# Performance work log

Hardware: AMD Instinct MI355X
Metric: run time of the kernel (lower is better)

Reference implementation:

```python
import jax, jax.numpy as jnp
import numpy as np
import math

C = 256
N_HEAD = 8
GROUPS = 16
EPS = 1e-5


def group_norm(x, w, b):
    # x: [B, C, H, W]; biased variance over (group_channels, H, W), like torch GroupNorm
    B, Cc, H, W = x.shape
    xg = x.reshape(B, GROUPS, Cc // GROUPS, H, W)
    mean = xg.mean(axis=(2, 3, 4), keepdims=True)
    var = ((xg - mean) ** 2).mean(axis=(2, 3, 4), keepdims=True)
    xn = ((xg - mean) * jax.lax.rsqrt(var + EPS)).reshape(B, Cc, H, W)
    return xn * w[None, :, None, None] + b[None, :, None, None]


def setup_inputs() -> dict:
    key = jax.random.key(0)
    k0, k1, k2, k3, k4, k5 = jax.random.split(key, 6)
    B, H, W = 4, 48, 48
    input_feat = jax.random.normal(k0, (B, C, H, W), dtype=jnp.float32)
    gn_weight = jnp.ones((C,), dtype=jnp.float32) + 0.02 * jax.random.normal(k1, (C,), dtype=jnp.float32)
    gn_bias = 0.02 * jax.random.normal(k2, (C,), dtype=jnp.float32)
    w_qkv = jax.random.normal(k3, (3 * C, C), dtype=jnp.float32) / math.sqrt(C)  # Conv2d 1x1, no bias
    w_out = jax.random.normal(k4, (C, C), dtype=jnp.float32) / math.sqrt(C)      # Conv2d 1x1
    b_out = 0.02 * jax.random.normal(k5, (C,), dtype=jnp.float32)
    return {"input_feat": input_feat, "gn_weight": gn_weight, "gn_bias": gn_bias,
            "w_qkv": w_qkv, "w_out": w_out, "b_out": b_out}


def reference(input_feat, gn_weight, gn_bias, w_qkv, w_out, b_out):
    # H=W=48 <= max_attn_size=48 -> full attention branch
    B, Cc, H, W = input_feat.shape
    n, d = N_HEAD, Cc // N_HEAD
    S = H * W
    normed = group_norm(input_feat, gn_weight, gn_bias)
    # 1x1 conv QKV: [B, 3C, H, W]
    qkv = jnp.einsum('oc,bchw->bohw', w_qkv, normed)
    # view(B, n, 3*d, H, W).chunk(3, dim=2) == reshape to (B, n, 3, d, S)
    qkv = qkv.reshape(B, n, 3, d, S)
    q, k, v = qkv[:, :, 0], qkv[:, :, 1], qkv[:, :, 2]  # each [B, n, d, S]
    # NOTE: original divides by sqrt(channel), not sqrt(head_dim)
    scale = 1.0 / math.sqrt(Cc)
    scores = jnp.einsum('bnds,bndt->bnst', q, k) * scale  # [B, n, S, S]
    attn = jax.nn.softmax(scores, axis=-1)
    o = jnp.einsum('bnst,bndt->bnds', attn, v)  # [B, n, d, S]
    o = o.reshape(B, Cc, H, W)
    out = jnp.einsum('oc,bchw->bohw', w_out, o) + b_out[None, :, None, None]
    return out + input_feat
```

## Files before the change

kernel.cpp:

```cpp
#include <hip/hip_runtime.h>
#include <hip/hip_bf16.h>
#include <stdint.h>

#define S    2304
#define CHN  256
#define BATCH 4
#define NKEYS 1152
#define QS   0.09016844005556021f

typedef __attribute__((ext_vector_type(8))) short bf16x8;
typedef __attribute__((ext_vector_type(4))) short bf16x4;
typedef __attribute__((ext_vector_type(4))) float f32x4;
typedef __attribute__((ext_vector_type(4))) uint32_t u32x4;
typedef __attribute__((ext_vector_type(4))) unsigned short u16x4;
typedef unsigned short u16;

#define AS1 __attribute__((address_space(1)))
#define AS3 __attribute__((address_space(3)))
#define GLDS(gptr, lptr) __builtin_amdgcn_global_load_lds((const AS1 void*)(gptr), (AS3 void*)(lptr), 16, 0, 0)

__device__ __forceinline__ u16 f2bf(float f) {
  union { float f; uint32_t u; } v; v.f = f;
  uint32_t u = v.u;
  u += 0x7fffu + ((u >> 16) & 1u);
  return (u16)(u >> 16);
}
__device__ __forceinline__ float bf2f(u16 h) {
  union { uint32_t u; float f; } v; v.u = ((uint32_t)h) << 16;
  return v.f;
}
__device__ __forceinline__ uint32_t pk_bf16(float a, float b) {
  union { __hip_bfloat162 h; uint32_t u; } cv;
  cv.h = __float22bfloat162_rn(make_float2(a, b));
  return cv.u;
}

__global__ void k_gnstats(const float* __restrict__ x,
                          const float* __restrict__ wq, const float* __restrict__ wo,
                          u16* __restrict__ wq_bf, u16* __restrict__ wo_bf,
                          float* __restrict__ sraw) {
  int blk = blockIdx.x;
  int bg = blk >> 2, part = blk & 3;
  const float4* p = (const float4*)(x + (size_t)bg * 36864) + part * 2304;
  float s = 0.f, ss = 0.f;
  for (int i = threadIdx.x; i < 2304; i += 256) {
    float4 v = p[i];
    s  += v.x + v.y + v.z + v.w;
    ss += v.x * v.x + v.y * v.y + v.z * v.z + v.w * v.w;
  }
  int lane = threadIdx.x & 63, wv = threadIdx.x >> 6;
  for (int m = 1; m < 64; m <<= 1) { s += __shfl_xor(s, m, 64); ss += __shfl_xor(ss, m, 64); }
  __shared__ float rs[4], rss[4];
  if (lane == 0) { rs[wv] = s; rss[wv] = ss; }
  __syncthreads();
  if (threadIdx.x == 0) {
    sraw[blk * 2]     = rs[0] + rs[1] + rs[2] + rs[3];
    sraw[blk * 2 + 1] = rss[0] + rss[1] + rss[2] + rss[3];
  }
  int gid = blk * 256 + threadIdx.x;
  #pragma unroll
  for (int it = 0; it < 3; ++it) {
    int i = gid + it * 65536;
    wq_bf[i] = f2bf(wq[i]);
  }
  wo_bf[gid] = f2bf(wo[gid]);
}

__global__ void k_gnnorm(const float* __restrict__ x, const float* __restrict__ w,
                         const float* __restrict__ bias, const float* __restrict__ sraw,
                         u16* __restrict__ nt) {
  int bid = blockIdx.x;
  int b = bid / 144, r = bid % 144;
  int sblk = r >> 2, cq = r & 3;
  int t = threadIdx.x;
  int ni = t & 63, cgrp = t >> 6;
  int s = sblk * 64 + ni;
  int cbase = cq * 64 + cgrp * 16;
  int bgi = b * 16 + (cbase >> 4);
  float sx  = sraw[bgi * 8]     + sraw[bgi * 8 + 2] + sraw[bgi * 8 + 4] + sraw[bgi * 8 + 6];
  float ssx = sraw[bgi * 8 + 1] + sraw[bgi * 8 + 3] + sraw[bgi * 8 + 5] + sraw[bgi * 8 + 7];
  float mean = sx * (1.f / 36864.f);
  float var  = ssx * (1.f / 36864.f) - mean * mean;
  float rstd = rsqrtf(var + 1e-5f);
  bf16x8 v0, v1;
  #pragma unroll
  for (int e = 0; e < 16; ++e) {
    int c = cbase + e;
    float val = x[(size_t)(b * 256 + c) * S + s];
    float xn = (val - mean) * rstd * w[c] + bias[c];
    if (e < 8) v0[e] = (short)f2bf(xn); else v1[e - 8] = (short)f2bf(xn);
  }
  u16* dst = nt + (size_t)(b * S + s) * 256 + cbase;
  *(bf16x8*)dst = v0;
  *(bf16x8*)(dst + 8) = v1;
}

__global__ __launch_bounds__(256) void k_qkv(const u16* __restrict__ A,
                                             const u16* __restrict__ Bm,
                                             u16* __restrict__ qkt,
                                             u16* __restrict__ vt) {
  __shared__ __align__(16) u16 As[2][64 * 32];
  __shared__ __align__(16) u16 Bs[2][128 * 32];
  int tid = threadIdx.x, lane = tid & 63, w = tid >> 6;
  int wr = w >> 1, wc = w & 1;
  int cb = lane & 15, q4 = lane >> 4;
  int m0 = blockIdx.y * 64, n0 = blockIdx.x * 128;

  const u16* gA0 = A  + (size_t)(m0 + (tid >> 2)) * 256 + (tid & 3) * 8;
  const u16* gB0 = Bm + (size_t)(n0 + (tid >> 2)) * 256 + (tid & 3) * 8;
  const u16* gB1 = gB0 + 64 * 256;
  char* lA = (char*)&As[0][0] + (w << 10);
  char* lB = (char*)&Bs[0][0] + (w << 10);

  #define STAGE_Q(buf, k0) do {                      \
    GLDS(gA0 + (k0), lA + (buf) * 4096);             \
    GLDS(gB0 + (k0), lB + (buf) * 8192);             \
    GLDS(gB1 + (k0), lB + (buf) * 8192 + 4096);      \
  } while (0)

  f32x4 zero4 = {0.f, 0.f, 0.f, 0.f};
  f32x4 acc[2][4];
  for (int i = 0; i < 2; ++i) for (int j = 0; j < 4; ++j) acc[i][j] = zero4;

  STAGE_Q(0, 0);
  __syncthreads();
  for (int ks = 0; ks < 8; ++ks) {
    int cur = ks & 1;
    if (ks < 7) STAGE_Q(cur ^ 1, (ks + 1) * 32);
    const u16* as = &As[cur][0];
    const u16* bs = &Bs[cur][0];
    bf16x8 af[2], bfr[4];
    for (int i = 0; i < 2; ++i)
      af[i]  = *(const bf16x8*)&as[(wr * 32 + i * 16 + cb) * 32 + 8 * q4];
    for (int j = 0; j < 4; ++j)
      bfr[j] = *(const bf16x8*)&bs[(wc * 64 + j * 16 + cb) * 32 + 8 * q4];
    for (int i = 0; i < 2; ++i)
      for (int j = 0; j < 4; ++j)
        acc[i][j] = __builtin_amdgcn_mfma_f32_16x16x32_bf16(af[i], bfr[j], acc[i][j], 0, 0, 0);
    __syncthreads();
  }

  for (int i = 0; i < 2; ++i)
    for (int j = 0; j < 4; ++j) {
      int ob = m0 + wr * 32 + i * 16 + q4 * 4;
      int n  = n0 + wc * 64 + j * 16 + cb;
      int h = ob / 96, oq = ob % 96;
      if (oq < 64) {
        float sc = (oq < 32) ? QS : 1.f;
        u16x4 pk;
        for (int r = 0; r < 4; ++r) pk[r] = f2bf(acc[i][j][r] * sc);
        *(u16x4*)&qkt[(size_t)n * 512 + h * 64 + oq] = pk;
      } else {
        int nk = n & 31;
        int np = (n & ~31) | ((((nk >> 2) & 3) << 3) + ((nk >> 4) << 2) + (nk & 3));
        for (int r = 0; r < 4; ++r)
          vt[(size_t)(h * 32 + oq - 64 + r) * 9216 + np] = f2bf(acc[i][j][r]);
      }
    }
  #undef STAGE_Q
}

__global__ __launch_bounds__(256, 4) void k_attn(const u16* __restrict__ qkt,
                                                 const u16* __restrict__ vt,
                                                 u16* __restrict__ ot) {
  __shared__ __align__(16) u16 Ks[2][2][2048];
  __shared__ __align__(16) u16 Vd[2][2][2048];

  int tid = threadIdx.x, lane = tid & 63, w = tid >> 6;
  int cb = lane & 15, g4 = lane >> 4;
  int qw = w & 1, half = w >> 1;
  int hw = blockIdx.x;
  int orig = (hw & 7) * 144 + (hw >> 3);
  int bh = orig / 36, qtile = orig % 36;
  int b = bh >> 3, h = bh & 7;
  int q0 = qtile * 64 + qw * 32;

  const u16* kbase = qkt + (size_t)(b * S) * 512 + h * 64 + 32 + (size_t)half * NKEYS * 512;
  const u16* vbase = vt + (size_t)(h * 32) * 9216 + (size_t)b * S + half * NKEYS;

  bf16x8 qf[2];
  #pragma unroll
  for (int qi = 0; qi < 2; ++qi)
    qf[qi] = *(const bf16x8*)&qkt[(size_t)(b * S + q0 + 16 * qi + cb) * 512 + h * 64 + 8 * g4];
  bf16x8 vones;
  #pragma unroll
  for (int e = 0; e < 8; ++e) vones[e] = (short)0x3F80;

  f32x4 zero4 = {0.f, 0.f, 0.f, 0.f};
  f32x4 acc_o[2][2];
  acc_o[0][0] = zero4; acc_o[0][1] = zero4; acc_o[1][0] = zero4; acc_o[1][1] = zero4;
  f32x4 lacc4[2]; lacc4[0] = zero4; lacc4[1] = zero4;

  int xk = (cb ^ (cb >> 2)) & 3;

  const u16* p_k = &Ks[half][0][cb * 32 + ((g4 ^ xk) * 8)];
  const u16* p_v[2];
  #pragma unroll
  for (int kk = 0; kk < 2; ++kk)
    p_v[kk] = &Vd[half][0][cb * 64 + (((4 * kk + g4) ^ (cb & 7)) << 3)];

  int ww = w & 1;
  int c1 = ww * 64 + lane, c2 = c1 + 128;
  int kr1 = c1 >> 2, kc1 = (c1 & 3) ^ ((kr1 ^ (kr1 >> 2)) & 3);
  int kr2 = c2 >> 2, kc2 = (c2 & 3) ^ ((kr2 ^ (kr2 >> 2)) & 3);
  int vr1 = c1 >> 3, vc1 = (c1 & 7) ^ (vr1 & 7);
  int vr2 = c2 >> 3, vc2 = (c2 & 7) ^ (vr2 & 7);
  const u16* gK1 = kbase + (size_t)kr1 * 512 + kc1 * 8;
  const u16* gK2 = kbase + (size_t)kr2 * 512 + kc2 * 8;
  const u16* gV1 = vbase + (size_t)vr1 * 9216 + vc1 * 8;
  const u16* gV2 = vbase + (size_t)vr2 * 9216 + vc2 * 8;
  char* ldsK = (char*)&Ks[half][0][0] + (ww << 10);
  char* ldsV = (char*)&Vd[half][0][0] + (ww << 10);

  #define STAGE_A(buf) do {                          \
    GLDS(gK1, ldsK + (buf) * 4096);                  \
    GLDS(gK2, ldsK + (buf) * 4096 + 2048);           \
    GLDS(gV1, ldsV + (buf) * 4096);                  \
    GLDS(gV2, ldsV + (buf) * 4096 + 2048);           \
    gK1 += 64 * 512; gK2 += 64 * 512;                \
    gV1 += 64; gV2 += 64;                            \
  } while (0)

  #define TILE(buf, pf) do {                                                   \
    if (pf) STAGE_A(buf ^ 1);                                                  \
    bf16x8 kf[4];                                                              \
    _Pragma("unroll")                                                          \
    for (int k4 = 0; k4 < 4; ++k4)                                             \
      kf[k4] = *(const bf16x8*)(p_k + (buf) * 2048 + k4 * 512);                \
    bf16x8 vb[2][2];                          \
    _Pragma("unroll")                                                          \
    for (int jd = 0; jd < 2; ++jd)                                             \
      _Pragma("unroll")                                                        \
      for (int kk = 0; kk < 2; ++kk)                                           \
        vb[jd][kk] = *(const bf16x8*)(p_v[kk] + (buf) * 2048 + jd * 1024);     \
    _Pragma("unroll")                                                          \
    for (int qi = 0; qi < 2; ++qi) {                                           \
      f32x4 pacc[4];                                                           \
      __builtin_amdgcn_s_setprio(1);                                           \
      _Pragma("unroll")                                                        \
      for (int k4 = 0; k4 < 4; ++k4)                                           \
        pacc[k4] = __builtin_amdgcn_mfma_f32_16x16x32_bf16(kf[k4], qf[qi], zero4, 0, 0, 0); \
      __builtin_amdgcn_s_setprio(0);                                           \
      uint32_t W01[4], W23[4];                                                 \
      _Pragma("unroll")                                                        \
      for (int k4 = 0; k4 < 4; ++k4) {                                         \
        f32x4 p = pacc[k4];                                                    \
        float e0 = __builtin_amdgcn_exp2f(p[0]);                               \
        float e1 = __builtin_amdgcn_exp2f(p[1]);                               \
        float e2 = __builtin_amdgcn_exp2f(p[2]);                               \
        float e3 = __builtin_amdgcn_exp2f(p[3]);                               \
        W01[k4] = pk_bf16(e0, e1);                                             \
        W23[k4] = pk_bf16(e2, e3);                                             \
      }                                                                        \
      union { u32x4 u; bf16x8 v; } pu0, pu1;                                   \
      pu0.u = (u32x4){W01[0], W23[0], W01[1], W23[1]};                         \
      pu1.u = (u32x4){W01[2], W23[2], W01[3], W23[3]};                         \
      __builtin_amdgcn_s_setprio(1);                                           \
      lacc4[qi] = __builtin_amdgcn_mfma_f32_16x16x32_bf16(pu0.v, vones, lacc4[qi], 0, 0, 0); \
      lacc4[qi] = __builtin_amdgcn_mfma_f32_16x16x32_bf16(pu1.v, vones, lacc4[qi], 0, 0, 0); \
      _Pragma("unroll")                                                        \
      for (int jd = 0; jd < 2; ++jd) {                                         \
        acc_o[qi][jd] = __builtin_amdgcn_mfma_f32_16x16x32_bf16(pu0.v, vb[jd][0], acc_o[qi][jd], 0, 0, 0); \
        acc_o[qi][jd] = __builtin_amdgcn_mfma_f32_16x16x32_bf16(pu1.v, vb[jd][1], acc_o[qi][jd], 0, 0, 0); \
      }                                                                        \
      __builtin_amdgcn_s_setprio(0);                                           \
    }                                                                          \
    __syncthreads();                                                           \
  } while (0)

  STAGE_A(0);
  __syncthreads();
  for (int it = 0; it < 9; ++it) {
    TILE(0, 1);
    TILE(1, it < 8);
  }

  float* scrK = (float*)&Ks[0][0][0];
  float* scrV = (float*)&Vd[0][0][0];
  float* LsF  = scrK + 3072;
  int reg = qw * 2 + half;
  float* myS = (reg < 2 ? scrK : scrV) + (reg & 1) * 1152;
  #pragma unroll
  for (int qi = 0; qi < 2; ++qi)
    #pragma unroll
    for (int jd = 0; jd < 2; ++jd)
      *(f32x4*)&myS[(cb + 16 * jd) * 36 + 16 * qi + 4 * g4] = acc_o[qi][jd];
  if (cb == 0) {
    *(f32x4*)&LsF[qw * 64 + half * 32 + 4 * g4] = lacc4[0];
    *(f32x4*)&LsF[qw * 64 + half * 32 + 16 + 4 * g4] = lacc4[1];
  }
  __syncthreads();

  const float* s0p = (qw == 0 ? scrK : scrV);
  const float* s1p = s0p + 1152;
  int dd = half * 16 + cb;
  #pragma unroll
  for (int qi2 = 0; qi2 < 2; ++qi2) {
    f32x4 s0 = *(const f32x4*)&s0p[dd * 36 + 16 * qi2 + 4 * g4];
    f32x4 s1 = *(const f32x4*)&s1p[dd * 36 + 16 * qi2 + 4 * g4];
    f32x4 lt0 = *(const f32x4*)&LsF[qw * 64 + 16 * qi2 + 4 * g4];
    f32x4 lt1 = *(const f32x4*)&LsF[qw * 64 + 32 + 16 * qi2 + 4 * g4];
    #pragma unroll
    for (int r = 0; r < 4; ++r) {
      float inv = __builtin_amdgcn_rcpf(lt0[r] + lt1[r]);
      int sq = q0 + 16 * qi2 + 4 * g4 + r;
      ot[(size_t)(b * S + sq) * 256 + h * 32 + dd] = f2bf((s0[r] + s1[r]) * inv);
    }
  }
  #undef STAGE_A
  #undef TILE
}

__global__ __launch_bounds__(256) void k_oproj(const u16* __restrict__ A,
                                               const u16* __restrict__ Bm,
                                               float* __restrict__ out,
                                               const float* __restrict__ bias,
                                               const float* __restrict__ resid) {
  __shared__ __align__(16) u16 As[2][64 * 32];
  __shared__ __align__(16) u16 Bs[2][64 * 32];
  int tid = threadIdx.x, lane = tid & 63, w = tid >> 6;
  int cb = lane & 15, q4 = lane >> 4;
  int m0 = blockIdx.y * 64, n0 = blockIdx.x * 64;

  const u16* gA0 = A  + (size_t)(m0 + (tid >> 2)) * 256 + (tid & 3) * 8;
  const u16* gB0 = Bm + (size_t)(n0 + (tid >> 2)) * 256 + (tid & 3) * 8;
  char* lA = (char*)&As[0][0] + (w << 10);
  char* lB = (char*)&Bs[0][0] + (w << 10);

  #define STAGE_O(buf, k0) do {                      \
    GLDS(gA0 + (k0), lA + (buf) * 4096);             \
    GLDS(gB0 + (k0), lB + (buf) * 4096);             \
  } while (0)

  f32x4 zero4 = {0.f, 0.f, 0.f, 0.f};
  f32x4 acc[4];
  for (int j = 0; j < 4; ++j) acc[j] = zero4;

  STAGE_O(0, 0);
  __syncthreads();
  for (int ks = 0; ks < 8; ++ks) {
    int cur = ks & 1;
    if (ks < 7) STAGE_O(cur ^ 1, (ks + 1) * 32);
    const u16* as = &As[cur][0];
    const u16* bs = &Bs[cur][0];
    bf16x8 af = *(const bf16x8*)&as[(w * 16 + cb) * 32 + 8 * q4];
    bf16x8 bfr[4];
    for (int j = 0; j < 4; ++j)
      bfr[j] = *(const bf16x8*)&bs[(j * 16 + cb) * 32 + 8 * q4];
    for (int j = 0; j < 4; ++j)
      acc[j] = __builtin_amdgcn_mfma_f32_16x16x32_bf16(af, bfr[j], acc[j], 0, 0, 0);
    __syncthreads();
  }

  for (int j = 0; j < 4; ++j)
    for (int r = 0; r < 4; ++r) {
      int o = m0 + w * 16 + q4 * 4 + r;
      int n = n0 + j * 16 + cb;
      int b = n / S, s2 = n % S;
      size_t gi = (size_t)(b * 256 + o) * S + s2;
      out[gi] = acc[j][r] + bias[o] + resid[gi];
    }
  #undef STAGE_O
}

extern "C" void kernel_launch(void* const* d_in, const int* in_sizes, int n_in,
                              void* d_out, int out_size, void* d_ws, size_t ws_size,
                              hipStream_t stream) {
  const float* input = (const float*)d_in[0];
  const float* gnw   = (const float*)d_in[1];
  const float* gnb   = (const float*)d_in[2];
  const float* wqkv  = (const float*)d_in[3];
  const float* wout  = (const float*)d_in[4];
  const float* bout  = (const float*)d_in[5];
  float* out = (float*)d_out;
  char* ws = (char*)d_ws;

  size_t o_wq  = 0;
  size_t o_wo  = o_wq + (size_t)768 * 256 * 2;
  size_t o_st  = o_wo + (size_t)256 * 256 * 2;
  size_t o_nt  = o_st + 2048;
  size_t o_qkt = o_nt + (size_t)9216 * 256 * 2;
  size_t o_vt  = o_qkt + (size_t)9216 * 512 * 2;

  u16*    wq_bf = (u16*)(ws + o_wq);
  u16*    wo_bf = (u16*)(ws + o_wo);
  float*  sraw  = (float*)(ws + o_st);
  u16*    nt    = (u16*)(ws + o_nt);
  u16*    qkt   = (u16*)(ws + o_qkt);
  u16*    vt    = (u16*)(ws + o_vt);
  u16*    otb   = (u16*)(ws + o_nt);

  k_gnstats<<<256, 256, 0, stream>>>(input, wqkv, wout, wq_bf, wo_bf, sraw);
  k_gnnorm<<<576, 256, 0, stream>>>(input, gnw, gnb, sraw, nt);
  k_qkv<<<dim3(72, 12), 256, 0, stream>>>(wq_bf, nt, qkt, vt);
  k_attn<<<1152, 256, 0, stream>>>(qkt, vt, otb);
  k_oproj<<<dim3(144, 4), 256, 0, stream>>>(wo_bf, otb, out, bout, input);
}
```

Baseline: 77.28 us.

## Double attention query tile per block and split GN stats over more blocks

The attention kernel now has each block process 128 queries (64 per wave pair) instead of 64, halving the grid to 576 blocks. Each K/V tile staged into LDS is therefore reused across twice as many queries, which cuts global K/V traffic. The cost is more accumulator registers and the removal of the occupancy hint of 4 from launch bounds. The combine scratch is now a union with a larger padded layout. Separately, the GroupNorm stats kernel is split across 1024 blocks (16 partials per group), and the normalize kernel sums all 16 partials.

```diff
diff --git a/kernel.cpp b/kernel.cpp
--- a/kernel.cpp
+++ b/kernel.cpp
@@ -40,10 +40,10 @@
                           u16* __restrict__ wq_bf, u16* __restrict__ wo_bf,
                           float* __restrict__ sraw) {
   int blk = blockIdx.x;
-  int bg = blk >> 2, part = blk & 3;
-  const float4* p = (const float4*)(x + (size_t)bg * 36864) + part * 2304;
+  int bg = blk >> 4, part = blk & 15;
+  const float4* p = (const float4*)(x + (size_t)bg * 36864) + part * 576;
   float s = 0.f, ss = 0.f;
-  for (int i = threadIdx.x; i < 2304; i += 256) {
+  for (int i = threadIdx.x; i < 576; i += 256) {
     float4 v = p[i];
     s  += v.x + v.y + v.z + v.w;
     ss += v.x * v.x + v.y * v.y + v.z * v.z + v.w * v.w;
@@ -58,12 +58,8 @@
     sraw[blk * 2 + 1] = rss[0] + rss[1] + rss[2] + rss[3];
   }
   int gid = blk * 256 + threadIdx.x;
-  #pragma unroll
-  for (int it = 0; it < 3; ++it) {
-    int i = gid + it * 65536;
-    wq_bf[i] = f2bf(wq[i]);
-  }
-  wo_bf[gid] = f2bf(wo[gid]);
+  if (gid < 196608) wq_bf[gid] = f2bf(wq[gid]);
+  if (gid < 65536)  wo_bf[gid] = f2bf(wo[gid]);
 }
 
 __global__ void k_gnnorm(const float* __restrict__ x, const float* __restrict__ w,
@@ -77,8 +73,12 @@
   int s = sblk * 64 + ni;
   int cbase = cq * 64 + cgrp * 16;
   int bgi = b * 16 + (cbase >> 4);
-  float sx  = sraw[bgi * 8]     + sraw[bgi * 8 + 2] + sraw[bgi * 8 + 4] + sraw[bgi * 8 + 6];
-  float ssx = sraw[bgi * 8 + 1] + sraw[bgi * 8 + 3] + sraw[bgi * 8 + 5] + sraw[bgi * 8 + 7];
+  float sx = 0.f, ssx = 0.f;
+  #pragma unroll
+  for (int pp = 0; pp < 16; ++pp) {
+    sx  += sraw[bgi * 32 + pp * 2];
+    ssx += sraw[bgi * 32 + pp * 2 + 1];
+  }
   float mean = sx * (1.f / 36864.f);
   float var  = ssx * (1.f / 36864.f) - mean * mean;
   float rstd = rsqrtf(var + 1e-5f);
@@ -160,46 +160,50 @@
   #undef STAGE_Q
 }
 
-__global__ __launch_bounds__(256, 4) void k_attn(const u16* __restrict__ qkt,
-                                                 const u16* __restrict__ vt,
-                                                 u16* __restrict__ ot) {
-  __shared__ __align__(16) u16 Ks[2][2][2048];
-  __shared__ __align__(16) u16 Vd[2][2][2048];
+struct SMain { u16 Ks[2][2][2048]; u16 Vd[2][2][2048]; };
+struct SComb { float O[4][2176]; float L[4][64]; };
+__global__ __launch_bounds__(256) void k_attn(const u16* __restrict__ qkt,
+                                              const u16* __restrict__ vt,
+                                              u16* __restrict__ ot) {
+  __shared__ __align__(16) union { SMain s; SComb c; } lds;
 
   int tid = threadIdx.x, lane = tid & 63, w = tid >> 6;
   int cb = lane & 15, g4 = lane >> 4;
   int qw = w & 1, half = w >> 1;
   int hw = blockIdx.x;
-  int orig = (hw & 7) * 144 + (hw >> 3);
-  int bh = orig / 36, qtile = orig % 36;
+  int orig = (hw & 7) * 72 + (hw >> 3);
+  int bh = orig / 18, qtile = orig % 18;
   int b = bh >> 3, h = bh & 7;
-  int q0 = qtile * 64 + qw * 32;
+  int q0 = qtile * 128 + qw * 64;
 
   const u16* kbase = qkt + (size_t)(b * S) * 512 + h * 64 + 32 + (size_t)half * NKEYS * 512;
   const u16* vbase = vt + (size_t)(h * 32) * 9216 + (size_t)b * S + half * NKEYS;
 
-  bf16x8 qf[2];
-  #pragma unroll
-  for (int qi = 0; qi < 2; ++qi)
+  bf16x8 qf[4];
+  #pragma unroll
+  for (int qi = 0; qi < 4; ++qi)
     qf[qi] = *(const bf16x8*)&qkt[(size_t)(b * S + q0 + 16 * qi + cb) * 512 + h * 64 + 8 * g4];
   bf16x8 vones;
   #pragma unroll
   for (int e = 0; e < 8; ++e) vones[e] = (short)0x3F80;
 
   f32x4 zero4 = {0.f, 0.f, 0.f, 0.f};
-  f32x4 acc_o[2][2];
-  acc_o[0][0] = zero4; acc_o[0][1] = zero4; acc_o[1][0] = zero4; acc_o[1][1] = zero4;
-  f32x4 lacc4[2]; lacc4[0] = zero4; lacc4[1] = zero4;
+  f32x4 acc_o[4][2];
+  #pragma unroll
+  for (int qi = 0; qi < 4; ++qi) { acc_o[qi][0] = zero4; acc_o[qi][1] = zero4; }
+  f32x4 lacc4[4];
+  #pragma unroll
+  for (int qi = 0; qi < 4; ++qi) lacc4[qi] = zero4;
 
   int xk = (cb ^ (cb >> 2)) & 3;
 
-  const u16* p_k = &Ks[half][0][cb * 32 + ((g4 ^ xk) * 8)];
+  const u16* p_k = &lds.s.Ks[half][0][cb * 32 + ((g4 ^ xk) * 8)];
   const u16* p_v[2];
   #pragma unroll
   for (int kk = 0; kk < 2; ++kk)
-    p_v[kk] = &Vd[half][0][cb * 64 + (((4 * kk + g4) ^ (cb & 7)) << 3)];
-
-  int ww = w & 1;
+    p_v[kk] = &lds.s.Vd[half][0][cb * 64 + (((4 * kk + g4) ^ (cb & 7)) << 3)];
+
+  int ww = qw;
   int c1 = ww * 64 + lane, c2 = c1 + 128;
   int kr1 = c1 >> 2, kc1 = (c1 & 3) ^ ((kr1 ^ (kr1 >> 2)) & 3);
   int kr2 = c2 >> 2, kc2 = (c2 & 3) ^ ((kr2 ^ (kr2 >> 2)) & 3);
@@ -209,8 +213,8 @@
   const u16* gK2 = kbase + (size_t)kr2 * 512 + kc2 * 8;
   const u16* gV1 = vbase + (size_t)vr1 * 9216 + vc1 * 8;
   const u16* gV2 = vbase + (size_t)vr2 * 9216 + vc2 * 8;
-  char* ldsK = (char*)&Ks[half][0][0] + (ww << 10);
-  char* ldsV = (char*)&Vd[half][0][0] + (ww << 10);
+  char* ldsK = (char*)&lds.s.Ks[half][0][0] + (ww << 10);
+  char* ldsV = (char*)&lds.s.Vd[half][0][0] + (ww << 10);
 
   #define STAGE_A(buf) do {                          \
     GLDS(gK1, ldsK + (buf) * 4096);                  \
@@ -227,14 +231,14 @@
     _Pragma("unroll")                                                          \
     for (int k4 = 0; k4 < 4; ++k4)                                             \
       kf[k4] = *(const bf16x8*)(p_k + (buf) * 2048 + k4 * 512);                \
-    bf16x8 vb[2][2];                          \
+    bf16x8 vb[2][2];                           \
     _Pragma("unroll")                                                          \
     for (int jd = 0; jd < 2; ++jd)                                             \
       _Pragma("unroll")                                                        \
       for (int kk = 0; kk < 2; ++kk)                                           \
         vb[jd][kk] = *(const bf16x8*)(p_v[kk] + (buf) * 2048 + jd * 1024);     \
     _Pragma("unroll")                                                          \
-    for (int qi = 0; qi < 2; ++qi) {                                           \
+    for (int qi = 0; qi < 4; ++qi) {                                           \
       f32x4 pacc[4];                                                           \
       __builtin_amdgcn_s_setprio(1);                                           \
       _Pragma("unroll")                                                        \
@@ -275,31 +279,29 @@
     TILE(1, it < 8);
   }
 
-  float* scrK = (float*)&Ks[0][0][0];
-  float* scrV = (float*)&Vd[0][0][0];
-  float* LsF  = scrK + 3072;
   int reg = qw * 2 + half;
-  float* myS = (reg < 2 ? scrK : scrV) + (reg & 1) * 1152;
-  #pragma unroll
-  for (int qi = 0; qi < 2; ++qi)
+  float* myO = lds.c.O[reg];
+  #pragma unroll
+  for (int qi = 0; qi < 4; ++qi)
     #pragma unroll
     for (int jd = 0; jd < 2; ++jd)
-      *(f32x4*)&myS[(cb + 16 * jd) * 36 + 16 * qi + 4 * g4] = acc_o[qi][jd];
+      *(f32x4*)&myO[(cb + 16 * jd) * 68 + 16 * qi + 4 * g4] = acc_o[qi][jd];
   if (cb == 0) {
-    *(f32x4*)&LsF[qw * 64 + half * 32 + 4 * g4] = lacc4[0];
-    *(f32x4*)&LsF[qw * 64 + half * 32 + 16 + 4 * g4] = lacc4[1];
+    #pragma unroll
+    for (int qi = 0; qi < 4; ++qi)
+      *(f32x4*)&lds.c.L[reg][16 * qi + 4 * g4] = lacc4[qi];
   }
   __syncthreads();
 
-  const float* s0p = (qw == 0 ? scrK : scrV);
-  const float* s1p = s0p + 1152;
+  const float* A0 = lds.c.O[qw * 2];
+  const float* A1 = lds.c.O[qw * 2 + 1];
   int dd = half * 16 + cb;
   #pragma unroll
-  for (int qi2 = 0; qi2 < 2; ++qi2) {
-    f32x4 s0 = *(const f32x4*)&s0p[dd * 36 + 16 * qi2 + 4 * g4];
-    f32x4 s1 = *(const f32x4*)&s1p[dd * 36 + 16 * qi2 + 4 * g4];
-    f32x4 lt0 = *(const f32x4*)&LsF[qw * 64 + 16 * qi2 + 4 * g4];
-    f32x4 lt1 = *(const f32x4*)&LsF[qw * 64 + 32 + 16 * qi2 + 4 * g4];
+  for (int qi2 = 0; qi2 < 4; ++qi2) {
+    f32x4 s0 = *(const f32x4*)&A0[dd * 68 + 16 * qi2 + 4 * g4];
+    f32x4 s1 = *(const f32x4*)&A1[dd * 68 + 16 * qi2 + 4 * g4];
+    f32x4 lt0 = *(const f32x4*)&lds.c.L[qw * 2][16 * qi2 + 4 * g4];
+    f32x4 lt1 = *(const f32x4*)&lds.c.L[qw * 2 + 1][16 * qi2 + 4 * g4];
     #pragma unroll
     for (int r = 0; r < 4; ++r) {
       float inv = __builtin_amdgcn_rcpf(lt0[r] + lt1[r]);
@@ -378,7 +380,7 @@
   size_t o_wq  = 0;
   size_t o_wo  = o_wq + (size_t)768 * 256 * 2;
   size_t o_st  = o_wo + (size_t)256 * 256 * 2;
-  size_t o_nt  = o_st + 2048;
+  size_t o_nt  = o_st + 8192;
   size_t o_qkt = o_nt + (size_t)9216 * 256 * 2;
   size_t o_vt  = o_qkt + (size_t)9216 * 512 * 2;
 
@@ -390,9 +392,9 @@
   u16*    vt    = (u16*)(ws + o_vt);
   u16*    otb   = (u16*)(ws + o_nt);
 
-  k_gnstats<<<256, 256, 0, stream>>>(input, wqkv, wout, wq_bf, wo_bf, sraw);
+  k_gnstats<<<1024, 256, 0, stream>>>(input, wqkv, wout, wq_bf, wo_bf, sraw);
   k_gnnorm<<<576, 256, 0, stream>>>(input, gnw, gnb, sraw, nt);
   k_qkv<<<dim3(72, 12), 256, 0, stream>>>(wq_bf, nt, qkt, vt);
-  k_attn<<<1152, 256, 0, stream>>>(qkt, vt, otb);
+  k_attn<<<576, 256, 0, stream>>>(qkt, vt, otb);
   k_oproj<<<dim3(144, 4), 256, 0, stream>>>(wo_bf, otb, out, bout, input);
 }
```

After: 91.58 us. 1.19x slower.
